# Performance work log

Hardware: AMD Instinct MI355X
Metric: run time of the kernel (lower is better)

## Reference

```python
import jax, jax.numpy as jnp
import numpy as np
import math

B, S, DIM, HEADS, HEAD_DIM = 2, 2048, 1024, 16, 64
ROT_DIM, ROPE_THETA = 64, 10000.0


def make_rope(seq_len):
    # DitRotary.forward: theta over half rotary_dim, duplicated interleaved pairs
    theta = 1.0 / (ROPE_THETA ** (np.arange(0, ROT_DIM, 2, dtype=np.float32) / ROT_DIM))
    pos = np.arange(seq_len, dtype=np.float32).reshape(-1, 1)
    idx = pos * theta  # [S, 32]
    cos = np.stack((np.cos(idx), np.cos(idx)), axis=-1).reshape(seq_len, -1)  # [S, 64]
    sin = np.stack((np.sin(idx), np.sin(idx)), axis=-1).reshape(seq_len, -1)
    # unsqueeze(2).unsqueeze(1) -> [1, S, 1, 64]
    return jnp.asarray(cos)[None, :, None, :], jnp.asarray(sin)[None, :, None, :]


def rotate_half(x):
    # interleaved-pair rotation: (x1, x2) -> (-x2, x1)
    x = x.reshape(*x.shape[:-1], -1, 2)
    x1, x2 = x[..., 0], x[..., 1]
    return jnp.stack((-x2, x1), axis=-1).reshape(*x.shape[:-2], -1)


def apply_rotary(x, cos, sin):
    return x * cos + rotate_half(x) * sin


def setup_inputs() -> dict:
    key = jax.random.key(0)
    ks = jax.random.split(key, 8)
    sc = 1.0 / math.sqrt(DIM)
    x = jax.random.normal(ks[0], (B, S, DIM), dtype=jnp.float32)
    cos, sin = make_rope(S)
    Wq = jax.random.normal(ks[1], (DIM, DIM), dtype=jnp.float32) * sc
    bq = jnp.zeros((DIM,), jnp.float32)
    Wk = jax.random.normal(ks[2], (DIM, DIM), dtype=jnp.float32) * sc
    bk = jnp.zeros((DIM,), jnp.float32)
    Wv = jax.random.normal(ks[3], (DIM, DIM), dtype=jnp.float32) * sc
    bv = jnp.zeros((DIM,), jnp.float32)
    Wo = jax.random.normal(ks[4], (DIM, DIM), dtype=jnp.float32) * sc
    bo = jnp.zeros((DIM,), jnp.float32)
    mask = jnp.ones((B, 1, 1, S), dtype=bool)
    return {"x": x, "cos": cos, "sin": sin, "Wq": Wq, "bq": bq, "Wk": Wk,
            "bk": bk, "Wv": Wv, "bv": bv, "Wo": Wo, "bo": bo, "mask": mask}


def reference(x, cos, sin, Wq, bq, Wk, bk, Wv, bv, Wo, bo, mask):
    b, s, _ = x.shape
    q = (x @ Wq.T + bq).reshape(b, s, HEADS, HEAD_DIM)
    k = (x @ Wk.T + bk).reshape(b, s, HEADS, HEAD_DIM)
    v = (x @ Wv.T + bv).reshape(b, s, HEADS, HEAD_DIM)
    # partial rotary: applied only to head index 0 (dim 2 of [B,S,H,D])
    q = jnp.concatenate([apply_rotary(q[:, :, :1, :], cos, sin), q[:, :, 1:, :]], axis=2)
    k = jnp.concatenate([apply_rotary(k[:, :, :1, :], cos, sin), k[:, :, 1:, :]], axis=2)
    # [B,H,S,D]
    q = q.transpose(0, 2, 1, 3)
    k = k.transpose(0, 2, 1, 3)
    v = v.transpose(0, 2, 1, 3)
    neg = jnp.finfo(jnp.float32).min
    attn_mask = jnp.where(mask, 0.0, neg)  # ~mask * finfo.min
    scores = jnp.einsum("bhsd,bhtd->bhst", q, k) / math.sqrt(HEAD_DIM)
    scores = scores + attn_mask
    probs = jax.nn.softmax(scores.astype(jnp.float32), axis=-1).astype(q.dtype)
    out = jnp.einsum("bhst,bhtd->bhsd", probs, v)
    out = out.transpose(0, 2, 1, 3).reshape(b, s, HEADS * HEAD_DIM)
    return out @ Wo.T + bo
```

## Files before the change

kernel.cpp:

```cpp
#include <hip/hip_runtime.h>
#include <hip/hip_bf16.h>


typedef __attribute__((ext_vector_type(8))) __bf16 bf16x8;
typedef __attribute__((ext_vector_type(4))) __bf16 bf16x4;
typedef __attribute__((ext_vector_type(4))) float f32x4;
typedef __attribute__((ext_vector_type(4))) short s16x4;

#define NB_B 2
#define NB_S 2048
#define NB_DIM 1024
#define NB_H 16
#define NB_HD 64
#define NB_BS (NB_B * NB_S)

__device__ __forceinline__ void async_cp16(const __bf16* g, __bf16* l) {
    __builtin_amdgcn_global_load_lds(
        (const __attribute__((address_space(1))) unsigned int*)g,
        (__attribute__((address_space(3))) unsigned int*)l, 16, 0, 0);
}

__global__ __launch_bounds__(256) void cvt_kernel(
    const float* __restrict__ x,  const float* __restrict__ wq,
    const float* __restrict__ wk, const float* __restrict__ wv,
    const float* __restrict__ wo,
    __bf16* __restrict__ xb,  __bf16* __restrict__ wqb,
    __bf16* __restrict__ wkb, __bf16* __restrict__ wvb,
    __bf16* __restrict__ wob) {
    const int XQ = (NB_BS * NB_DIM) / 4;
    const int WQ = (NB_DIM * NB_DIM) / 4;
    int i = blockIdx.x * 256 + threadIdx.x;
    const float* src; __bf16* dst; int off;
    if (i < XQ)              { src = x;  dst = xb;  off = i; }
    else if (i < XQ + WQ)    { src = wq; dst = wqb; off = i - XQ; }
    else if (i < XQ + 2*WQ)  { src = wk; dst = wkb; off = i - XQ - WQ; }
    else if (i < XQ + 3*WQ)  { src = wv; dst = wvb; off = i - XQ - 2*WQ; }
    else                     { src = wo; dst = wob; off = i - XQ - 3*WQ; }
    f32x4 v = *(const f32x4*)(src + (size_t)off * 4);
    bf16x4 b;
#pragma unroll
    for (int j = 0; j < 4; ++j) b[j] = (__bf16)v[j];
    *(bf16x4*)(dst + (size_t)off * 4) = b;
}

__global__ __launch_bounds__(256) void gemm_qkv_kernel(
    const __bf16* __restrict__ A,
    const float* __restrict__ cosb, const float* __restrict__ sinb,
    const __bf16* __restrict__ Wq, const float* __restrict__ bq, __bf16* __restrict__ qbuf,
    const __bf16* __restrict__ Wk, const float* __restrict__ bk, __bf16* __restrict__ kbuf,
    const __bf16* __restrict__ Wv, const float* __restrict__ bv, __bf16* __restrict__ vtbuf) {
    constexpr int K = 1024;
    __shared__ __align__(16) __bf16 As[128][32];
    __shared__ __align__(16) __bf16 Bs[128][32];

    const int z = blockIdx.z;
    const __bf16* W; const float* bias;
    if (z == 0)      { W = Wq; bias = bq; }
    else if (z == 1) { W = Wk; bias = bk; }
    else             { W = Wv; bias = bv; }

    const int tid = threadIdx.x;
    const int lane = tid & 63;
    const int w = tid >> 6;
    const int wm = w >> 1, wn = w & 1;
    const int row16 = lane & 15, quad = lane >> 4;
    const int m0 = blockIdx.x * 128, n0 = blockIdx.y * 128;

    f32x4 acc[4][4] = {};

    for (int kt = 0; kt < K; kt += 32) {
        __syncthreads();
#pragma unroll
        for (int i = 0; i < 2; ++i) {
            int c = tid + i * 256;
            int row = c >> 2;
            int co = (c & 3) << 3;
            async_cp16(A + (size_t)(m0 + row) * K + kt + co, &As[row][co]);
            async_cp16(W + (size_t)(n0 + row) * K + kt + co, &Bs[row][co]);
        }
        __syncthreads();

        bf16x8 af[4], bf[4];
#pragma unroll
        for (int t = 0; t < 4; ++t) {
            af[t] = *(const bf16x8*)&As[wm * 64 + t * 16 + row16][quad * 8];
            bf[t] = *(const bf16x8*)&Bs[wn * 64 + t * 16 + row16][quad * 8];
        }
#pragma unroll
        for (int mt = 0; mt < 4; ++mt)
#pragma unroll
            for (int nt = 0; nt < 4; ++nt)
                acc[mt][nt] = __builtin_amdgcn_mfma_f32_16x16x32_bf16(af[mt], bf[nt], acc[mt][nt], 0, 0, 0);
    }

    if (z == 2) {
#pragma unroll
        for (int mt = 0; mt < 4; ++mt) {
            int row = m0 + wm * 64 + mt * 16 + quad * 4;
            int b = row >> 11, s = row & (NB_S - 1);
#pragma unroll
            for (int nt = 0; nt < 4; ++nt) {
                int col = n0 + wn * 64 + nt * 16 + row16;
                float bv = bias[col];
                bf16x4 pack;
#pragma unroll
                for (int r = 0; r < 4; ++r) pack[r] = (__bf16)(acc[mt][nt][r] + bv);
                *(bf16x4*)&vtbuf[(size_t)b * (NB_DIM * NB_S) + (size_t)col * NB_S + s] = pack;
            }
        }
    } else {
        __bf16* C = (z == 0) ? qbuf : kbuf;
        const bool rope = (n0 == 0) && (wn == 0);
#pragma unroll
        for (int mt = 0; mt < 4; ++mt) {
            int row = m0 + wm * 64 + mt * 16 + quad * 4;
#pragma unroll
            for (int nt = 0; nt < 4; ++nt) {
                int col = n0 + wn * 64 + nt * 16 + row16;
                float bv = bias[col];
#pragma unroll
                for (int r = 0; r < 4; ++r) {
                    float val = acc[mt][nt][r] + bv;
                    if (rope) {
                        float part = __shfl_xor(val, 1, 64);
                        int srow = (row + r) & (NB_S - 1);
                        float c  = cosb[srow * 64 + col];
                        float sn = sinb[srow * 64 + col];
                        val = (lane & 1) ? (val * c + part * sn) : (val * c - part * sn);
                    }
                    C[(size_t)(row + r) * NB_DIM + col] = (__bf16)val;
                }
            }
        }
    }
}

__global__ __launch_bounds__(256) void gemm_o_kernel(
    const __bf16* __restrict__ A, const __bf16* __restrict__ W,
    const float* __restrict__ bias, float* __restrict__ C) {
    constexpr int K = 1024;
    __shared__ __align__(16) __bf16 As[128][32];
    __shared__ __align__(16) __bf16 Bs[64][32];

    const int tid = threadIdx.x;
    const int lane = tid & 63;
    const int w = tid >> 6;
    const int row16 = lane & 15, quad = lane >> 4;
    const int m0 = blockIdx.x * 128, n0 = blockIdx.y * 64;

    f32x4 acc[2][4] = {};

    for (int kt = 0; kt < K; kt += 32) {
        __syncthreads();
#pragma unroll
        for (int i = 0; i < 2; ++i) {
            int c = tid + i * 256;
            int row = c >> 2;
            int co = (c & 3) << 3;
            async_cp16(A + (size_t)(m0 + row) * K + kt + co, &As[row][co]);
        }
        {
            int row = tid >> 2;
            int co = (tid & 3) << 3;
            async_cp16(W + (size_t)(n0 + row) * K + kt + co, &Bs[row][co]);
        }
        __syncthreads();

        bf16x8 af[2], bf[4];
#pragma unroll
        for (int t = 0; t < 2; ++t)
            af[t] = *(const bf16x8*)&As[w * 32 + t * 16 + row16][quad * 8];
#pragma unroll
        for (int nt = 0; nt < 4; ++nt)
            bf[nt] = *(const bf16x8*)&Bs[nt * 16 + row16][quad * 8];
#pragma unroll
        for (int mt = 0; mt < 2; ++mt)
#pragma unroll
            for (int nt = 0; nt < 4; ++nt)
                acc[mt][nt] = __builtin_amdgcn_mfma_f32_16x16x32_bf16(af[mt], bf[nt], acc[mt][nt], 0, 0, 0);
    }

#pragma unroll
    for (int mt = 0; mt < 2; ++mt) {
        int row = m0 + w * 32 + mt * 16 + quad * 4;
#pragma unroll
        for (int nt = 0; nt < 4; ++nt) {
            int col = n0 + nt * 16 + row16;
            float bv = bias[col];
#pragma unroll
            for (int r = 0; r < 4; ++r)
                C[(size_t)(row + r) * NB_DIM + col] = acc[mt][nt][r] + bv;
        }
    }
}

__global__ __launch_bounds__(256) void attn_kernel(const __bf16* __restrict__ qb,
                                                   const __bf16* __restrict__ kb,
                                                   const __bf16* __restrict__ vtb,
                                                   __bf16* __restrict__ ob) {
    __shared__ __align__(16) __bf16 Ks[128][72];
    __shared__ __align__(16) __bf16 Vts[64][132];

    const int tid = threadIdx.x;
    const int lane = tid & 63;
    const int w = tid >> 6;
    const int row16 = lane & 15, quad = lane >> 4;
    const int bh = blockIdx.y;
    const int b = bh >> 4, h = bh & 15;
    const int q0 = blockIdx.x * 128 + w * 32;

    const size_t headoff = (size_t)b * NB_S * NB_DIM + (size_t)h * NB_HD;
    const size_t vtoff = (size_t)b * (NB_DIM * NB_S) + (size_t)(h * NB_HD) * NB_S;

    const float qscale = 0.18033688011112042f;
    bf16x8 qf[2][2];
#pragma unroll
    for (int m = 0; m < 2; ++m)
#pragma unroll
        for (int hh = 0; hh < 2; ++hh) {
            bf16x8 v = *(const bf16x8*)(qb + headoff + (size_t)(q0 + m * 16 + row16) * NB_DIM + hh * 32 + quad * 8);
#pragma unroll
            for (int j = 0; j < 8; ++j) v[j] = (__bf16)((float)v[j] * qscale);
            qf[m][hh] = v;
        }

    f32x4 o[2][4] = {};
    f32x4 ol[2] = {};

    const short one_bf16 = (short)0x3F80;
    const s16x4 onesf = {one_bf16, one_bf16, one_bf16, one_bf16};

    bf16x8 kreg[4], vreg[4];
#pragma unroll
    for (int i = 0; i < 4; ++i) {
        int c = tid + i * 256;
        kreg[i] = *(const bf16x8*)(kb + headoff + (size_t)(c >> 3) * NB_DIM + ((c & 7) << 3));
        vreg[i] = *(const bf16x8*)(vtb + vtoff + (size_t)(c >> 4) * NB_S + ((c & 15) << 3));
    }

    for (int kt = 0; kt < 16; ++kt) {
        __syncthreads();
#pragma unroll
        for (int i = 0; i < 4; ++i) {
            int c = tid + i * 256;
            *(bf16x8*)&Ks[c >> 3][(c & 7) << 3] = kreg[i];
            bf16x4 lo, hi;
#pragma unroll
            for (int j = 0; j < 4; ++j) { lo[j] = vreg[i][j]; hi[j] = vreg[i][j + 4]; }
            *(bf16x4*)&Vts[c >> 4][(c & 15) << 3] = lo;
            *(bf16x4*)&Vts[c >> 4][((c & 15) << 3) + 4] = hi;
        }
        __syncthreads();
        if (kt < 15) {
            int base = (kt + 1) * 128;
#pragma unroll
            for (int i = 0; i < 4; ++i) {
                int c = tid + i * 256;
                kreg[i] = *(const bf16x8*)(kb + headoff + (size_t)(base + (c >> 3)) * NB_DIM + ((c & 7) << 3));
                vreg[i] = *(const bf16x8*)(vtb + vtoff + (size_t)(c >> 4) * NB_S + base + ((c & 15) << 3));
            }
        }

        s16x4 pf[2][8];
#pragma unroll
        for (int t = 0; t < 8; ++t) {
            f32x4 s0 = {}, s1 = {};
            __builtin_amdgcn_s_setprio(1);
#pragma unroll
            for (int hh = 0; hh < 2; ++hh) {
                bf16x8 kf = *(const bf16x8*)&Ks[t * 16 + row16][hh * 32 + quad * 8];
                s0 = __builtin_amdgcn_mfma_f32_16x16x32_bf16(kf, qf[0][hh], s0, 0, 0, 0);
                s1 = __builtin_amdgcn_mfma_f32_16x16x32_bf16(kf, qf[1][hh], s1, 0, 0, 0);
            }
            __builtin_amdgcn_s_setprio(0);
            bf16x4 p0, p1;
#pragma unroll
            for (int r = 0; r < 4; ++r) {
                float e0 = __builtin_amdgcn_exp2f(s0[r]); p0[r] = (__bf16)e0;
                float e1 = __builtin_amdgcn_exp2f(s1[r]); p1[r] = (__bf16)e1;
            }
            pf[0][t] = __builtin_bit_cast(s16x4, p0);
            pf[1][t] = __builtin_bit_cast(s16x4, p1);
            ol[0] = __builtin_amdgcn_mfma_f32_16x16x16bf16_1k(pf[0][t], onesf, ol[0], 0, 0, 0);
            ol[1] = __builtin_amdgcn_mfma_f32_16x16x16bf16_1k(pf[1][t], onesf, ol[1], 0, 0, 0);
        }

        __builtin_amdgcn_s_setprio(1);
#pragma unroll
        for (int nt = 0; nt < 4; ++nt)
#pragma unroll
            for (int t = 0; t < 8; ++t) {
                s16x4 vf = *(const s16x4*)&Vts[nt * 16 + row16][t * 16 + quad * 4];
                o[0][nt] = __builtin_amdgcn_mfma_f32_16x16x16bf16_1k(pf[0][t], vf, o[0][nt], 0, 0, 0);
                o[1][nt] = __builtin_amdgcn_mfma_f32_16x16x16bf16_1k(pf[1][t], vf, o[1][nt], 0, 0, 0);
            }
        __builtin_amdgcn_s_setprio(0);
    }

#pragma unroll
    for (int m = 0; m < 2; ++m)
#pragma unroll
        for (int r = 0; r < 4; ++r) {
            float inv = 1.f / ol[m][r];
            int row = q0 + m * 16 + quad * 4 + r;
#pragma unroll
            for (int nt = 0; nt < 4; ++nt)
                ob[headoff + (size_t)row * NB_DIM + nt * 16 + row16] = (__bf16)(o[m][nt][r] * inv);
        }
}

extern "C" void kernel_launch(void* const* d_in, const int* in_sizes, int n_in,
                              void* d_out, int out_size, void* d_ws, size_t ws_size,
                              hipStream_t stream) {
    const float* x    = (const float*)d_in[0];
    const float* cosb = (const float*)d_in[1];
    const float* sinb = (const float*)d_in[2];
    const float* Wq   = (const float*)d_in[3];
    const float* bq   = (const float*)d_in[4];
    const float* Wk   = (const float*)d_in[5];
    const float* bk   = (const float*)d_in[6];
    const float* Wv   = (const float*)d_in[7];
    const float* bv   = (const float*)d_in[8];
    const float* Wo   = (const float*)d_in[9];
    const float* bo   = (const float*)d_in[10];

    __bf16* qbuf  = (__bf16*)d_ws;
    __bf16* kbuf  = qbuf + (size_t)NB_BS * NB_DIM;
    __bf16* vtbuf = kbuf + (size_t)NB_BS * NB_DIM;
    __bf16* abuf  = vtbuf + (size_t)NB_BS * NB_DIM;
    __bf16* xb    = abuf + (size_t)NB_BS * NB_DIM;
    __bf16* wqb   = xb + (size_t)NB_BS * NB_DIM;
    __bf16* wkb   = wqb + (size_t)NB_DIM * NB_DIM;
    __bf16* wvb   = wkb + (size_t)NB_DIM * NB_DIM;
    __bf16* wob   = wvb + (size_t)NB_DIM * NB_DIM;

    const int XQ = (NB_BS * NB_DIM) / 4, WQ = (NB_DIM * NB_DIM) / 4;
    cvt_kernel<<<(XQ + 4 * WQ) / 256, 256, 0, stream>>>(x, Wq, Wk, Wv, Wo,
                                                        xb, wqb, wkb, wvb, wob);

    dim3 gqkv(NB_BS / 128, NB_DIM / 128, 3);
    gemm_qkv_kernel<<<gqkv, 256, 0, stream>>>(xb, cosb, sinb,
                                              wqb, bq, qbuf,
                                              wkb, bk, kbuf,
                                              wvb, bv, vtbuf);

    attn_kernel<<<dim3(NB_S / 128, NB_B * NB_H), 256, 0, stream>>>(qbuf, kbuf, vtbuf, abuf);

    dim3 go(NB_BS / 128, NB_DIM / 64);
    gemm_o_kernel<<<go, 256, 0, stream>>>(abuf, wob, bo, (float*)d_out);
}
```

Measured before the change: 207.4 us.

## Triple-buffer LDS staging with async prefetch in QKV and output GEMMs

Both projection GEMMs drop the load-then-sync-then-compute loop with its two barriers per k-step. They now use a three-stage LDS ring that prefetches two k-tiles ahead, using explicit vmcnt waits and a single barrier per iteration. MFMA sections are wrapped in s_setprio to favour matrix issue. This aims to hide global-to-LDS latency behind compute, at the cost of triple the shared memory per block, which may lower occupancy.

```diff
diff --git a/kernel.cpp b/kernel.cpp
--- a/kernel.cpp
+++ b/kernel.cpp
@@ -50,8 +50,9 @@
     const __bf16* __restrict__ Wk, const float* __restrict__ bk, __bf16* __restrict__ kbuf,
     const __bf16* __restrict__ Wv, const float* __restrict__ bv, __bf16* __restrict__ vtbuf) {
     constexpr int K = 1024;
-    __shared__ __align__(16) __bf16 As[128][32];
-    __shared__ __align__(16) __bf16 Bs[128][32];
+    constexpr int NT = K / 32;
+    __shared__ __align__(16) __bf16 As[3][128][32];
+    __shared__ __align__(16) __bf16 Bs[3][128][32];
 
     const int z = blockIdx.z;
     const __bf16* W; const float* bias;
@@ -68,30 +69,46 @@
 
     f32x4 acc[4][4] = {};
 
-    for (int kt = 0; kt < K; kt += 32) {
-        __syncthreads();
+    auto stage = [&](int nb, int kt) {
 #pragma unroll
         for (int i = 0; i < 2; ++i) {
             int c = tid + i * 256;
             int row = c >> 2;
             int co = (c & 3) << 3;
-            async_cp16(A + (size_t)(m0 + row) * K + kt + co, &As[row][co]);
-            async_cp16(W + (size_t)(n0 + row) * K + kt + co, &Bs[row][co]);
-        }
-        __syncthreads();
-
-        bf16x8 af[4], bf[4];
+            async_cp16(A + (size_t)(m0 + row) * K + kt + co, &As[nb][row][co]);
+            async_cp16(W + (size_t)(n0 + row) * K + kt + co, &Bs[nb][row][co]);
+        }
+    };
+    auto compute = [&](int nb) {
+        bf16x8 af[4], bfr[4];
 #pragma unroll
         for (int t = 0; t < 4; ++t) {
-            af[t] = *(const bf16x8*)&As[wm * 64 + t * 16 + row16][quad * 8];
-            bf[t] = *(const bf16x8*)&Bs[wn * 64 + t * 16 + row16][quad * 8];
-        }
+            af[t]  = *(const bf16x8*)&As[nb][wm * 64 + t * 16 + row16][quad * 8];
+            bfr[t] = *(const bf16x8*)&Bs[nb][wn * 64 + t * 16 + row16][quad * 8];
+        }
+        __builtin_amdgcn_s_setprio(1);
 #pragma unroll
         for (int mt = 0; mt < 4; ++mt)
 #pragma unroll
             for (int nt = 0; nt < 4; ++nt)
-                acc[mt][nt] = __builtin_amdgcn_mfma_f32_16x16x32_bf16(af[mt], bf[nt], acc[mt][nt], 0, 0, 0);
-    }
+                acc[mt][nt] = __builtin_amdgcn_mfma_f32_16x16x32_bf16(af[mt], bfr[nt], acc[mt][nt], 0, 0, 0);
+        __builtin_amdgcn_s_setprio(0);
+    };
+
+    stage(0, 0);
+    stage(1, 32);
+    int cu = 0, pfb = 2;
+    for (int t = 0; t < NT - 1; ++t) {
+        asm volatile("s_waitcnt vmcnt(4)" ::: "memory");
+        __builtin_amdgcn_s_barrier();
+        if (t + 2 < NT) stage(pfb, (t + 2) * 32);
+        compute(cu);
+        cu  = (cu  == 2) ? 0 : cu + 1;
+        pfb = (pfb == 2) ? 0 : pfb + 1;
+    }
+    asm volatile("s_waitcnt vmcnt(0)" ::: "memory");
+    __builtin_amdgcn_s_barrier();
+    compute(cu);
 
     if (z == 2) {
 #pragma unroll
@@ -139,8 +156,9 @@
     const __bf16* __restrict__ A, const __bf16* __restrict__ W,
     const float* __restrict__ bias, float* __restrict__ C) {
     constexpr int K = 1024;
-    __shared__ __align__(16) __bf16 As[128][32];
-    __shared__ __align__(16) __bf16 Bs[64][32];
+    constexpr int NT = K / 32;
+    __shared__ __align__(16) __bf16 As[3][128][32];
+    __shared__ __align__(16) __bf16 Bs[3][64][32];
 
     const int tid = threadIdx.x;
     const int lane = tid & 63;
@@ -150,35 +168,51 @@
 
     f32x4 acc[2][4] = {};
 
-    for (int kt = 0; kt < K; kt += 32) {
-        __syncthreads();
+    auto stage = [&](int nb, int kt) {
 #pragma unroll
         for (int i = 0; i < 2; ++i) {
             int c = tid + i * 256;
             int row = c >> 2;
             int co = (c & 3) << 3;
-            async_cp16(A + (size_t)(m0 + row) * K + kt + co, &As[row][co]);
+            async_cp16(A + (size_t)(m0 + row) * K + kt + co, &As[nb][row][co]);
         }
         {
             int row = tid >> 2;
             int co = (tid & 3) << 3;
-            async_cp16(W + (size_t)(n0 + row) * K + kt + co, &Bs[row][co]);
-        }
-        __syncthreads();
-
-        bf16x8 af[2], bf[4];
+            async_cp16(W + (size_t)(n0 + row) * K + kt + co, &Bs[nb][row][co]);
+        }
+    };
+    auto compute = [&](int nb) {
+        bf16x8 af[2], bfr[4];
 #pragma unroll
         for (int t = 0; t < 2; ++t)
-            af[t] = *(const bf16x8*)&As[w * 32 + t * 16 + row16][quad * 8];
+            af[t] = *(const bf16x8*)&As[nb][w * 32 + t * 16 + row16][quad * 8];
 #pragma unroll
         for (int nt = 0; nt < 4; ++nt)
-            bf[nt] = *(const bf16x8*)&Bs[nt * 16 + row16][quad * 8];
+            bfr[nt] = *(const bf16x8*)&Bs[nb][nt * 16 + row16][quad * 8];
+        __builtin_amdgcn_s_setprio(1);
 #pragma unroll
         for (int mt = 0; mt < 2; ++mt)
 #pragma unroll
             for (int nt = 0; nt < 4; ++nt)
-                acc[mt][nt] = __builtin_amdgcn_mfma_f32_16x16x32_bf16(af[mt], bf[nt], acc[mt][nt], 0, 0, 0);
-    }
+                acc[mt][nt] = __builtin_amdgcn_mfma_f32_16x16x32_bf16(af[mt], bfr[nt], acc[mt][nt], 0, 0, 0);
+        __builtin_amdgcn_s_setprio(0);
+    };
+
+    stage(0, 0);
+    stage(1, 32);
+    int cu = 0, pfb = 2;
+    for (int t = 0; t < NT - 1; ++t) {
+        asm volatile("s_waitcnt vmcnt(3)" ::: "memory");
+        __builtin_amdgcn_s_barrier();
+        if (t + 2 < NT) stage(pfb, (t + 2) * 32);
+        compute(cu);
+        cu  = (cu  == 2) ? 0 : cu + 1;
+        pfb = (pfb == 2) ? 0 : pfb + 1;
+    }
+    asm volatile("s_waitcnt vmcnt(0)" ::: "memory");
+    __builtin_amdgcn_s_barrier();
+    compute(cu);
 
 #pragma unroll
     for (int mt = 0; mt < 2; ++mt) {
```

Result: slower. 211.6 us (+2.1%).
